# Kernel optimization log

Measured on AMD Instinct MI355X. Metric: run time of the kernel, lower is better.

The kernel has to match this reference:

```python
import jax, jax.numpy as jnp
import numpy as np

# Model dims (see init_kwargs / shape_source)
ROWS, COLS, C, K, L = 16, 16, 16, 3, 2
B, T = 16, 128
D = ROWS * COLS * C  # state_dim = 4096
PAD = (K - 1) // 2


def setup_inputs() -> dict:
    key = jax.random.key(0)
    ks = jax.random.split(key, 1 + 5 * L)
    inp = {"x_flat": jax.random.normal(ks[0], (B, T, ROWS * COLS), jnp.float32)}
    ki = 1
    for l in range(L):
        cin = (1 if l == 0 else C) + C  # conv sees concat(input, h)
        inp[f"conv_w{l}"] = jax.random.normal(ks[ki], (4 * C, cin, K), jnp.float32) * float(1.0 / np.sqrt(cin * K)); ki += 1
        inp[f"conv_b{l}"] = jnp.zeros((4 * C,), jnp.float32)
        s = float(1.0 / np.sqrt(D))
        inp[f"wq{l}"] = jax.random.normal(ks[ki], (D, D), jnp.float32) * s; ki += 1
        inp[f"wk{l}"] = jax.random.normal(ks[ki], (D, D), jnp.float32) * s; ki += 1
        inp[f"wv{l}"] = jax.random.normal(ks[ki], (D, D), jnp.float32) * s; ki += 1
        inp[f"wo{l}"] = jax.random.normal(ks[ki], (2 * D, D), jnp.float32) * float(1.0 / np.sqrt(2 * D)); ki += 1
    return inp


def _cell_step(x, h, c, cw, cb):
    # x: (B, ROWS, cin_x, COLS); h, c: (B, ROWS, C, COLS). Row-shared Conv1d
    # along cols over concat(x, h) -> 4C gates (standard ConvLSTM).
    z = jnp.concatenate([x, h], axis=2)
    z = z.reshape(B * ROWS, z.shape[2], COLS)
    g = jax.lax.conv_general_dilated(
        z, cw, window_strides=(1,), padding=[(PAD, PAD)],
        dimension_numbers=("NCH", "OIH", "NCH"))
    g = g.reshape(B, ROWS, 4 * C, COLS) + cb[None, None, :, None]
    i, f, gg, o = jnp.split(g, 4, axis=2)
    c_new = jax.nn.sigmoid(f) * c + jax.nn.sigmoid(i) * jnp.tanh(gg)
    h_new = jax.nn.sigmoid(o) * jnp.tanh(c_new)
    return h_new, c_new


def _attn_step(h_vec, kbuf, vbuf, step, wq, wo):
    # Causal dot-product attention: query from raw state, keys from raw
    # history, values from refined history (projections cached in kbuf/vbuf).
    q = h_vec @ wq                                        # (B, D)
    scores = jnp.einsum("bd,tbd->bt", q, kbuf) * (1.0 / np.sqrt(D))
    mask = (jnp.arange(T)[None, :] < step)                # (1, T) strictly-past
    scores = jnp.where(mask, scores, -1e30)
    m = jnp.max(scores, axis=1, keepdims=True)
    e = jnp.exp(scores - m) * mask
    w = e / jnp.maximum(e.sum(axis=1, keepdims=True), 1e-9)
    ctx = jnp.einsum("bt,tbd->bd", w, vbuf)               # zeros at step 0
    out = jnp.tanh(jnp.concatenate([h_vec, ctx], axis=1) @ wo)
    return out, w


def _forward(x_flat, layer_params):
    # frames: (T, B, ROWS, 1, COLS) -- matches torch view+unsqueeze(3)
    x = x_flat.reshape(B, T, ROWS, 1, COLS).transpose(1, 0, 2, 3, 4)
    h0 = tuple(jnp.zeros((B, ROWS, C, COLS), x_flat.dtype) for _ in range(L))
    kb0 = tuple(jnp.zeros((T, B, D), x_flat.dtype) for _ in range(L))

    def body(carry, x_t):
        hs, cs, kbs, vbs, s = carry
        inp = x_t
        nh, nc, nk, nv = [], [], [], []
        out = None
        for l in range(L):
            cw, cb, wq, wk, wv, wo = layer_params[l]
            h_raw, c_new = _cell_step(inp, hs[l], cs[l], cw, cb)
            h_vec = h_raw.reshape(B, D)
            out, _w = _attn_step(h_vec, kbs[l], vbs[l], s, wq, wo)
            nk.append(kbs[l].at[s].set(h_vec @ wk))   # append raw key
            nv.append(vbs[l].at[s].set(out @ wv))     # append refined value
            nh.append(h_raw); nc.append(c_new)
            inp = out.reshape(B, ROWS, C, COLS)
        return (tuple(nh), tuple(nc), tuple(nk), tuple(nv), s + 1), out

    init = (h0, h0, kb0, kb0, jnp.int32(0))
    _, outs = jax.lax.scan(body, init, x)
    return outs.transpose(1, 0, 2)  # (B, T, D) encoder outputs


def reference(x_flat, conv_w0, conv_b0, wq0, wk0, wv0, wo0,
              conv_w1, conv_b1, wq1, wk1, wv1, wo1):
    layer_params = [
        (conv_w0, conv_b0, wq0, wk0, wv0, wo0),
        (conv_w1, conv_b1, wq1, wk1, wv1, wo1),
    ]
    return _forward(x_flat, layer_params)
```

## Files before the change

### kernel.cpp

```cpp
#include <hip/hip_runtime.h>

typedef unsigned short u16;
typedef unsigned int u32;
typedef __attribute__((ext_vector_type(8))) short short8v;
typedef __attribute__((ext_vector_type(4))) float f32x4;
typedef __attribute__((ext_vector_type(8))) u16 ush8;
typedef __attribute__((ext_vector_type(4))) u16 ush4;

__device__ __forceinline__ u16 f2bf(float x) {
  u32 u = __builtin_bit_cast(u32, x);
  return (u16)((u + 0x7FFFu + ((u >> 16) & 1u)) >> 16);
}
__device__ __forceinline__ float bf2f(u16 h) {
  u32 u = ((u32)h) << 16;
  return __builtin_bit_cast(float, u);
}
__device__ __forceinline__ float sigm(float x) { return 1.f / (1.f + expf(-x)); }

typedef const __attribute__((address_space(1))) void gv_t;
typedef __attribute__((address_space(3))) void lv_t;
__device__ __forceinline__ void gload16(const void* g, void* l) {
  __builtin_amdgcn_global_load_lds((gv_t*)g, (lv_t*)l, 16, 0, 0);
}

__device__ __forceinline__ u32 ldsc32(const u32* p) {
  u32 v;
  asm volatile("global_load_dword %0, %1, off sc0 sc1\n\ts_waitcnt vmcnt(0)"
               : "=v"(v) : "v"(p) : "memory");
  return v;
}
__device__ __forceinline__ void atomswap32(u32* p, u32 v) {
  asm volatile("global_atomic_swap %0, %1, off" :: "v"(p), "v"(v) : "memory");
}

__global__ __launch_bounds__(256) void k_conv(int cin, int xmode,
    const float* __restrict__ xin, const float* __restrict__ cw,
    const float* __restrict__ cb, u16* __restrict__ hhi, u16* __restrict__ hlo)
{
  __shared__ float zb[32 * 18];
  __shared__ __align__(16) float wb[6144];
  __shared__ float bb[64];
  const int tid = threadIdx.x;
  const int b = blockIdx.x >> 4, r = blockIdx.x & 15;
  const int ch = tid >> 4, col = tid & 15;
  const int cx = cin - 16;
  for (int i = tid; i < 64 * cin * 3; i += 256) {
    int tap = i % 3, tmp = i / 3;
    int ic = tmp % cin, oc = tmp / cin;
    wb[(((oc & 15) * cin + ic) * 3 + tap) * 4 + (oc >> 4)] = cw[i];
  }
  if (tid < 64) bb[tid] = cb[tid];
  for (int i = tid; i < cin * 18; i += 256) zb[i] = 0.f;
  __syncthreads();
  float h = 0.f, c = 0.f;
  const int lane = tid & 63;
  for (int t = 0; t < 128; ++t) {
    if (xmode == 0) {
      if (ch == 0) zb[col + 1] = xin[((long)b * 128 + t) * 256 + r * 16 + col];
    } else {
      zb[ch * 18 + col + 1] = xin[((long)t * 16 + b) * 4096 + r * 256 + ch * 16 + col];
    }
    zb[(cx + ch) * 18 + col + 1] = h;
    __syncthreads();
    float a0 = bb[ch], a1 = bb[16 + ch], a2 = bb[32 + ch], a3 = bb[48 + ch];
    for (int ic = 0; ic < cin; ++ic) {
      float z1 = zb[ic * 18 + col + 1];
      float z0 = __shfl(z1, lane - 1);
      float z2 = __shfl(z1, lane + 1);
      if (col == 0) z0 = 0.f;
      if (col == 15) z2 = 0.f;
      const float4* wp = (const float4*)&wb[(ch * cin + ic) * 12];
      float4 w0 = wp[0], w1 = wp[1], w2 = wp[2];
      a0 += z0 * w0.x + z1 * w1.x + z2 * w2.x;
      a1 += z0 * w0.y + z1 * w1.y + z2 * w2.y;
      a2 += z0 * w0.z + z1 * w1.z + z2 * w2.z;
      a3 += z0 * w0.w + z1 * w1.w + z2 * w2.w;
    }
    __syncthreads();
    c = sigm(a1) * c + sigm(a0) * tanhf(a2);
    h = sigm(a3) * tanhf(c);
    long idx = ((long)t * 16 + b) * 4096 + (long)r * 256 + ch * 16 + col;
    u16 hh = f2bf(h);
    hhi[idx] = hh;
    hlo[idx] = f2bf(h - bf2f(hh));
  }
}

__global__ __launch_bounds__(256) void k_tsplit3(
    const float* __restrict__ W0, const float* __restrict__ W1,
    const float* __restrict__ W2, u16* __restrict__ hi, u16* __restrict__ lo)
{
  __shared__ float tb[32][33];
  const int y = blockIdx.y;
  const float* W = (y == 0) ? W0 : (y == 1) ? W1 : W2;
  u16* hid = hi + (unsigned long)y * 16777216UL;
  u16* lod = lo + (unsigned long)y * 16777216UL;
  const int tn = blockIdx.x & 127, tk = blockIdx.x >> 7;
  const int n0 = tn * 32, k0 = tk * 32;
  const int lr = threadIdx.x >> 5, lc = threadIdx.x & 31;
  #pragma unroll
  for (int i = 0; i < 4; ++i)
    tb[lr + i * 8][lc] = W[(long)(k0 + lr + i * 8) * 4096 + n0 + lc];
  __syncthreads();
  #pragma unroll
  for (int i = 0; i < 4; ++i) {
    int n = lr + i * 8;
    float v = tb[lc][n];
    long idx = (long)(n0 + n) * 4096 + k0 + lc;
    u16 h = f2bf(v);
    hid[idx] = h;
    lod[idx] = f2bf(v - bf2f(h));
  }
}

__global__ __launch_bounds__(256) void k_tsplit(const float* __restrict__ W,
    u16* __restrict__ hi, u16* __restrict__ lo)
{
  __shared__ float tb[32][33];
  const int tn = blockIdx.x & 127, tk = blockIdx.x >> 7;
  const int n0 = tn * 32, k0 = tk * 32;
  const int lr = threadIdx.x >> 5, lc = threadIdx.x & 31;
  #pragma unroll
  for (int i = 0; i < 4; ++i)
    tb[lr + i * 8][lc] = W[(long)(k0 + lr + i * 8) * 4096 + n0 + lc];
  __syncthreads();
  #pragma unroll
  for (int i = 0; i < 4; ++i) {
    int n = lr + i * 8;
    float v = tb[lc][n];
    long idx = (long)(n0 + n) * 4096 + k0 + lc;
    u16 h = f2bf(v);
    hi[idx] = h;
    lo[idx] = f2bf(v - bf2f(h));
  }
}

__global__ __launch_bounds__(256) void k_split(const float* __restrict__ W,
    u16* __restrict__ hi, u16* __restrict__ lo)
{
  long i = ((long)blockIdx.x * 256 + threadIdx.x) * 4;
  const float4 v = *(const float4*)&W[i];
  u16 h0 = f2bf(v.x), h1 = f2bf(v.y), h2 = f2bf(v.z), h3 = f2bf(v.w);
  ush4 hv = {h0, h1, h2, h3};
  ush4 lv = {f2bf(v.x - bf2f(h0)), f2bf(v.y - bf2f(h1)),
             f2bf(v.z - bf2f(h2)), f2bf(v.w - bf2f(h3))};
  *(ush4*)&hi[i] = hv;
  *(ush4*)&lo[i] = lv;
}

__global__ __launch_bounds__(256) void k_scores(
    const u16* __restrict__ Ahi, long lda, long aBS,
    const u16* __restrict__ Bhi, long ldb, long bBS,
    float* __restrict__ Sp)
{
  __shared__ __align__(16) u16 lds[2][16384];
  const int tid = threadIdx.x;
  const int lane = tid & 63;
  const int wv = tid >> 6;
  const long aOff = (long)blockIdx.y * aBS;
  const long bOff = (long)blockIdx.y * bBS;
  const long cOff = (long)blockIdx.y * 16384 + (long)blockIdx.z * 262144;
  const int kbase = blockIdx.z * 512;

  const int l8 = lane >> 3;
  const int cslot = (lane & 7) ^ l8;
  const int ck = (cslot & 3) * 8;
  const u16* aSrc = Ahi + aOff + (wv * 32 + l8) * lda + ck;
  const u16* bSrc = Bhi + bOff + (wv * 32 + l8) * ldb + ck;
  const int ldsAo = wv * 2048;
  const int ldsBo = 8192 + wv * 2048;

  const int r15 = lane & 15, kq = lane >> 4;
  const int s7 = r15 & 7;
  const int oHi = (kq ^ s7) * 8;
  const int aQ = (wv >> 1) * 64;
  const int bQ = (wv & 1) * 64;

  f32x4 acc[4][4] = {};

#define STAGE(buf, kofs)                                                     \
  {                                                                          \
    const u16* sa = aSrc + (kofs);                                           \
    const u16* sb = bSrc + (kofs);                                           \
    u16* la = &lds[buf][ldsAo];                                              \
    u16* lb = &lds[buf][ldsBo];                                              \
    gload16(sa,            la);        gload16(sa +  8 * lda, la + 512);     \
    gload16(sa + 16 * lda, la + 1024); gload16(sa + 24 * lda, la + 1536);    \
    gload16(sb,            lb);        gload16(sb +  8 * ldb, lb + 512);     \
    gload16(sb + 16 * ldb, lb + 1024); gload16(sb + 24 * ldb, lb + 1536);    \
  }

  STAGE(0, kbase)
  __syncthreads();
  int cur = 0;
  for (int k0 = kbase; k0 < kbase + 512; k0 += 32) {
    if (k0 + 32 < kbase + 512) STAGE(cur ^ 1, k0 + 32)
    const u16* L = &lds[cur][0];
    short8v bh[4];
    #pragma unroll
    for (int j = 0; j < 4; ++j)
      bh[j] = *(const short8v*)&L[8192 + (bQ + j * 16 + r15) * 64 + oHi];
    #pragma unroll
    for (int i = 0; i < 4; ++i) {
      short8v ah = *(const short8v*)&L[(aQ + i * 16 + r15) * 64 + oHi];
      #pragma unroll
      for (int j = 0; j < 4; ++j)
        acc[i][j] = __builtin_amdgcn_mfma_f32_16x16x32_bf16(ah, bh[j], acc[i][j], 0, 0, 0);
    }
    __syncthreads();
    cur ^= 1;
  }
#undef STAGE
  const long row0 = aQ, col0 = bQ;
  #pragma unroll
  for (int i = 0; i < 4; ++i)
    #pragma unroll
    for (int j = 0; j < 4; ++j) {
      long rr = row0 + i * 16 + kq * 4;
      long cc = col0 + j * 16 + r15;
      #pragma unroll
      for (int g = 0; g < 4; ++g)
        Sp[cOff + (rr + g) * 128 + cc] = acc[i][j][g];
    }
}

template<int NM, bool LOOUT>
__global__ __launch_bounds__(512) void k_gemm256(
    const u16* __restrict__ Ahi, const u16* __restrict__ Alo,
    const u16* __restrict__ Bhi, const u16* __restrict__ Blo,
    u16* __restrict__ Chi, u16* __restrict__ Clo, long ldc, int nTc)
{
  __shared__ __align__(16) u16 lds[73728];
  const int tid = threadIdx.x, lane = tid & 63, wv = tid >> 6;
  const int nwg = gridDim.x;
  const int bid2 = (blockIdx.x & 7) * (nwg >> 3) + (blockIdx.x >> 3);
  const int nT = bid2 % nTc, mT = bid2 / nTc;
  const long aRow0 = (long)mT * 256, bRow0 = (long)nT * 128;

  const int l8 = lane >> 3, cslot = (lane & 7) ^ l8, ck = (cslot & 3) * 8;
  const u16* aSrc = ((cslot < 4) ? Ahi : Alo) + (aRow0 + wv * 32 + l8) * 4096 + ck;
  const u16* bSrc = ((cslot < 4) ? Bhi : Blo) + (bRow0 + wv * 16 + l8) * 4096 + ck;
  const int laO = wv * 2048;
  const int lbO = 16384 + wv * 1024;

  const int r15 = lane & 15, kq = lane >> 4, s7 = r15 & 7;
  const int oHi = (kq ^ s7) * 8, oLo = ((4 + kq) ^ s7) * 8;
  const int wm = wv >> 1, wn = wv & 1;
  f32x4 acc[4][4] = {};

#define STG(buf, kofs)                                                       \
  {                                                                          \
    const u16* sa = aSrc + (kofs);                                           \
    const u16* sb = bSrc + (kofs);                                           \
    u16* la = &lds[(buf) * 24576 + laO];                                     \
    u16* lb = &lds[(buf) * 24576 + lbO];                                     \
    gload16(sa,             la);       gload16(sa +  8 * 4096, la + 512);    \
    gload16(sa + 16 * 4096, la + 1024); gload16(sa + 24 * 4096, la + 1536);  \
    gload16(sb,             lb);       gload16(sb +  8 * 4096, lb + 512);    \
  }

  STG(0, 0) STG(1, 32)
  for (int kt = 0; kt < 128; ++kt) {
    if (kt < 127) { asm volatile("s_waitcnt vmcnt(6)" ::: "memory"); }
    else          { asm volatile("s_waitcnt vmcnt(0)" ::: "memory"); }
    __builtin_amdgcn_sched_barrier(0);
    __builtin_amdgcn_s_barrier();
    const int bb = (kt % 3) * 24576;
    if (kt < 126) STG((kt + 2) % 3, (kt + 2) * 32)
    short8v ah[4], al[4], bh[4], bl[4];
    #pragma unroll
    for (int j = 0; j < 4; ++j) {
      int rb = bb + 16384 + (wn * 64 + j * 16 + r15) * 64;
      bh[j] = *(const short8v*)&lds[rb + oHi];
      if (NM >= 3) bl[j] = *(const short8v*)&lds[rb + oLo];
    }
    #pragma unroll
    for (int i = 0; i < 4; ++i) {
      int ra = bb + (wm * 64 + i * 16 + r15) * 64;
      ah[i] = *(const short8v*)&lds[ra + oHi];
      if (NM >= 2) al[i] = *(const short8v*)&lds[ra + oLo];
    }
    #pragma unroll
    for (int i = 0; i < 4; ++i)
      #pragma unroll
      for (int j = 0; j < 4; ++j) {
        acc[i][j] = __builtin_amdgcn_mfma_f32_16x16x32_bf16(ah[i], bh[j], acc[i][j], 0, 0, 0);
        if (NM >= 3) acc[i][j] = __builtin_amdgcn_mfma_f32_16x16x32_bf16(ah[i], bl[j], acc[i][j], 0, 0, 0);
        if (NM >= 2) acc[i][j] = __builtin_amdgcn_mfma_f32_16x16x32_bf16(al[i], bh[j], acc[i][j], 0, 0, 0);
      }
  }
#undef STG
  const long row0 = aRow0 + wm * 64;
  const long col0 = bRow0 + wn * 64;
  #pragma unroll
  for (int i = 0; i < 4; ++i)
    #pragma unroll
    for (int j = 0; j < 4; ++j) {
      long rr = row0 + i * 16 + kq * 4;
      long cc = col0 + j * 16 + r15;
      #pragma unroll
      for (int g = 0; g < 4; ++g) {
        float v = acc[i][j][g];
        long idx = (rr + g) * ldc + cc;
        u16 h = f2bf(v);
        Chi[idx] = h;
        if (LOOUT) Clo[idx] = f2bf(v - bf2f(h));
      }
    }
}

__global__ __launch_bounds__(256) void k_softmax(const float* __restrict__ Sp,
    float* __restrict__ Wx, u32* __restrict__ flags, u32* __restrict__ rel)
{
  if (blockIdx.x == 0) atomswap32(&flags[threadIdx.x * 16], 0);
  if (blockIdx.x == 1) atomswap32(&rel[threadIdx.x * 16], 0);
  const int wv = threadIdx.x >> 6, lane = threadIdx.x & 63;
  const int idx = blockIdx.x * 4 + wv;
  const int b = idx >> 7, t = idx & 127;
  const float* row = &Sp[(long)idx * 128];
  float s0 = 0.f, s1 = 0.f;
  #pragma unroll
  for (int s = 0; s < 8; ++s) {
    s0 += row[s * 262144 + lane];
    s1 += row[s * 262144 + lane + 64];
  }
  float v0 = (lane < t) ? s0 * 0.015625f : -1e30f;
  float v1 = (lane + 64 < t) ? s1 * 0.015625f : -1e30f;
  float m = fmaxf(v0, v1);
  #pragma unroll
  for (int off = 32; off; off >>= 1) m = fmaxf(m, __shfl_xor(m, off));
  float e0 = (lane < t) ? expf(v0 - m) : 0.f;
  float e1 = (lane + 64 < t) ? expf(v1 - m) : 0.f;
  float s = e0 + e1;
  #pragma unroll
  for (int off = 32; off; off >>= 1) s += __shfl_xor(s, off);
  float inv = 1.f / fmaxf(s, 1e-9f);
  float* wr = &Wx[((long)t * 16 + b) * 128];
  wr[lane] = e0 * inv;
  wr[lane + 64] = e1 * inv;
}

__global__ __launch_bounds__(512) void k_phaseC(
    const u16* __restrict__ Wvh, const u16* __restrict__ Wvl,
    const float* __restrict__ Wx,
    const u16* __restrict__ hoh, const u16* __restrict__ hol,
    u16* __restrict__ ring_h,
    float* __restrict__ fdest, int dmode,
    u32* __restrict__ flags, u32* __restrict__ rel)
{
  __shared__ float VO_lds[128 * 256];
  __shared__ float vo_w[8][256];
  __shared__ float pctx[2][256];
  const int tid = threadIdx.x;
  const int lane = tid & 63, wv = tid >> 6;
  const int n0 = blockIdx.x * 16;
  const int r15 = lane & 15, kq = lane >> 4;
  const long kb = (long)wv * 512 + kq * 8;

  short8v Bh[16], Bl[16];
  {
    const u16* bh = Wvh + (long)(n0 + r15) * 4096 + kb;
    const u16* bl = Wvl + (long)(n0 + r15) * 4096 + kb;
    #pragma unroll
    for (int c = 0; c < 16; ++c) {
      Bh[c] = *(const short8v*)(bh + c * 32);
      Bl[c] = *(const short8v*)(bl + c * 32);
    }
    #pragma unroll
    for (int c = 0; c < 16; ++c) {
      asm volatile("" : "+v"(Bh[c]));
      asm volatile("" : "+v"(Bl[c]));
    }
  }
  const long abase = (long)r15 * 4096 + kb;
  const int b8 = tid >> 4, col8 = tid & 15;

#define GBAR(n)                                                              \
  {                                                                          \
    asm volatile("s_waitcnt vmcnt(0)" ::: "memory");                         \
    __syncthreads();                                                         \
    if (tid == 0) {                                                          \
      atomswap32(&flags[(u32)blockIdx.x * 16], (n));                         \
      asm volatile("s_waitcnt vmcnt(0)" ::: "memory");                       \
    }                                                                        \
    if (blockIdx.x == 0) {                                                   \
      if (tid < 256) {                                                       \
        while (ldsc32(&flags[tid * 16]) < (n)) __builtin_amdgcn_s_sleep(1);  \
      }                                                                      \
      __syncthreads();                                                       \
      if (tid < 256) atomswap32(&rel[tid * 16], (n));                        \
    } else if (tid == 0) {                                                   \
      while (ldsc32(&rel[(u32)blockIdx.x * 16]) < (n))                       \
        __builtin_amdgcn_s_sleep(1);                                         \
    }                                                                        \
    __syncthreads();                                                         \
  }

#define RING_STORE(slot, oval)                                               \
  {                                                                          \
    u16 hh_ = f2bf(oval);                                                    \
    u32 vh_ = hh_;                                                           \
    u32 ph_ = (u32)__shfl_xor((int)vh_, 1);                                  \
    if (!(col8 & 1)) {                                                       \
      long oi_ = (long)(slot) * 65536 + (long)b8 * 4096 + n0 + col8;         \
      atomswap32((u32*)&ring_h[oi_], vh_ | (ph_ << 16));                     \
    }                                                                        \
  }

  if (tid < 256) {
    float v = tanhf(bf2f(hoh[(long)b8 * 12288 + n0 + col8])
                  + bf2f(hol[(long)b8 * 12288 + n0 + col8]));
    RING_STORE(0, v)
    if (dmode == 0) fdest[(long)b8 * 4096 + n0 + col8] = v;
    else            fdest[(long)b8 * 128 * 4096 + n0 + col8] = v;
  }
  u32 bn = 1;
  GBAR(bn) ++bn;

#define MF(a, b) acc = __builtin_amdgcn_mfma_f32_16x16x32_bf16(a, b, acc, 0, 0, 0);

  for (int t = 0; t < 127; ++t) {
    const u16* ph = ring_h + (long)t * 65536 + abase;
    short8v xh[16];
    #pragma unroll
    for (int c = 0; c < 16; ++c) xh[c] = *(const short8v*)(ph + c * 32);
    {
      const int p = tid >> 8, id = tid & 255;
      const int bm = id >> 4;
      const float* wrowm = &Wx[((long)(t + 1) * 16 + bm) * 128];
      float ctx = 0.f;
      for (int tp = p; tp < t; tp += 2)
        ctx += wrowm[tp] * VO_lds[tp * 256 + id];
      pctx[p][id] = ctx;
    }
    f32x4 acc = {0.f, 0.f, 0.f, 0.f};
    #pragma unroll
    for (int c = 0; c < 16; ++c) { MF(xh[c], Bh[c]) MF(xh[c], Bl[c]) }
    #pragma unroll
    for (int g = 0; g < 4; ++g)
      vo_w[wv][(kq * 4 + g) * 16 + r15] = acc[g];
    __syncthreads();
    if (tid < 256) {
      float v = vo_w[0][tid] + vo_w[1][tid] + vo_w[2][tid] + vo_w[3][tid]
              + vo_w[4][tid] + vo_w[5][tid] + vo_w[6][tid] + vo_w[7][tid];
      VO_lds[t * 256 + tid] = v;
      const float* wrow = &Wx[((long)(t + 1) * 16 + b8) * 128];
      long hix = ((long)(t + 1) * 16 + b8) * 12288 + n0 + col8;
      float o = tanhf(bf2f(hoh[hix]) + bf2f(hol[hix])
                      + pctx[0][tid] + pctx[1][tid] + wrow[t] * v);
      RING_STORE(t + 1, o)
      if (dmode == 0) fdest[((long)(t + 1) * 16 + b8) * 4096 + n0 + col8] = o;
      else            fdest[((long)b8 * 128 + (t + 1)) * 4096 + n0 + col8] = o;
    }
    if (t < 126) { GBAR(bn) ++bn; }
  }
#undef GBAR
#undef RING_STORE
#undef MF
}

extern "C" void kernel_launch(void* const* d_in, const int* in_sizes, int n_in,
                              void* d_out, int out_size, void* d_ws, size_t ws_size,
                              hipStream_t stream)
{
  (void)in_sizes; (void)n_in; (void)out_size;
  if (ws_size < 472383488UL) return;
  char* ws = (char*)d_ws;
  u16* WT_hi = (u16*)(ws + 0UL);
  u16* WT_lo = (u16*)(ws + 100663296UL);
  u16* WV_hi = (u16*)(ws + 33554432UL);
  u16* WV_lo = (u16*)(ws + 134217728UL);
  u16* QKOh  = (u16*)(ws + 201326592UL);
  u16* QKOl  = (u16*)(ws + 251658240UL);
  u16* Wvo_hi = (u16*)(ws + 301989888UL);
  u16* Wvo_lo = (u16*)(ws + 335544320UL);
  u16* Hs_hi = (u16*)(ws + 369098752UL);
  u16* Hs_lo = (u16*)(ws + 385875968UL);
  float* Wmx  = (float*)(ws + 403701760UL);
  float* OUT0 = (float*)(ws + 404754432UL);
  u16* ring_h = (u16*)(ws + 438308864UL);
  float* Sp   = (float*)(ws + 455086080UL);
  u32* flg    = (u32*)(ws + 471859200UL);
  u32* rel    = (u32*)(ws + 471875584UL);
  float* dout = (float*)d_out;
  const float* x_flat = (const float*)d_in[0];

  for (int l = 0; l < 2; ++l) {
    const float* cw = (const float*)d_in[1 + l * 6];
    const float* cb = (const float*)d_in[2 + l * 6];
    const float* wq = (const float*)d_in[3 + l * 6];
    const float* wk = (const float*)d_in[4 + l * 6];
    const float* wv = (const float*)d_in[5 + l * 6];
    const float* wo = (const float*)d_in[6 + l * 6];
    const int cin = (l == 0) ? 17 : 32;

    hipLaunchKernelGGL(k_conv, dim3(256), dim3(256), 0, stream,
        cin, l, (l == 0) ? x_flat : OUT0, cw, cb, Hs_hi, Hs_lo);

    hipLaunchKernelGGL(k_tsplit3, dim3(16384, 3), dim3(256), 0, stream,
        wq, wk, wo, WT_hi, WT_lo);
    hipLaunchKernelGGL((k_gemm256<1, false>), dim3(512), dim3(512), 0, stream,
        Hs_hi, Hs_hi, WT_hi, WT_hi, QKOh, (u16*)nullptr, 12288L, 64);
    hipLaunchKernelGGL((k_gemm256<3, true>), dim3(256), dim3(512), 0, stream,
        Hs_hi, Hs_lo, WT_hi + 33554432UL, WT_lo + 33554432UL,
        QKOh + 8192, QKOl + 8192, 12288L, 32);

    hipLaunchKernelGGL(k_tsplit, dim3(16384), dim3(256), 0, stream,
        wo + 16777216UL, WT_hi, WT_lo);
    hipLaunchKernelGGL(k_split, dim3(16384), dim3(256), 0, stream, wv, WV_hi, WV_lo);
    hipLaunchKernelGGL((k_gemm256<2, true>), dim3(512), dim3(512), 0, stream,
        WT_hi, WT_lo, WV_hi, WV_hi, Wvo_hi, Wvo_lo, 4096L, 32);

    hipLaunchKernelGGL(k_scores, dim3(1, 16, 8), dim3(256), 0, stream,
        QKOh, 12288L, 196608L, QKOh + 4096, 12288L, 196608L, Sp);
    hipLaunchKernelGGL(k_softmax, dim3(512), dim3(256), 0, stream, Sp, Wmx, flg, rel);

    hipLaunchKernelGGL(k_phaseC, dim3(256), dim3(512), 0, stream,
        Wvo_hi, Wvo_lo, Wmx, QKOh + 8192, QKOl + 8192,
        ring_h, (l == 0) ? OUT0 : dout, l, flg, rel);
  }
}
```

Before: 4.559 ms.

## Flatten grid barrier, overlap context reduction with barrier wait, merge prep kernels

The two-level grid barrier (every block signals, block 0 gathers and then broadcasts a release flag) is replaced with an all-to-all scheme in which each block polls all 256 flags directly. While the lower half of the threads spin on those flags, the upper half computes the attention context sum over past steps, moving that work off the critical path after the barrier. The wo transpose-split and wv split are also merged into one launch. The flat barrier adds polling traffic across all blocks, and the context sum now runs on only 256 threads instead of 512.

Measured after the change: 4.083 ms. 1.12x faster.

```diff
diff --git a/kernel.cpp b/kernel.cpp
--- a/kernel.cpp
+++ b/kernel.cpp
@@ -113,16 +113,29 @@
   }
 }
 
-__global__ __launch_bounds__(256) void k_tsplit(const float* __restrict__ W,
-    u16* __restrict__ hi, u16* __restrict__ lo)
-{
+__global__ __launch_bounds__(256) void k_prepB2(
+    const float* __restrict__ Woc, const float* __restrict__ Wv,
+    u16* __restrict__ thi, u16* __restrict__ tlo,
+    u16* __restrict__ vhi, u16* __restrict__ vlo)
+{
+  if (blockIdx.y == 1) {
+    long i = ((long)blockIdx.x * 256 + threadIdx.x) * 4;
+    const float4 v = *(const float4*)&Wv[i];
+    u16 h0 = f2bf(v.x), h1 = f2bf(v.y), h2 = f2bf(v.z), h3 = f2bf(v.w);
+    ush4 hv = {h0, h1, h2, h3};
+    ush4 lv = {f2bf(v.x - bf2f(h0)), f2bf(v.y - bf2f(h1)),
+               f2bf(v.z - bf2f(h2)), f2bf(v.w - bf2f(h3))};
+    *(ush4*)&vhi[i] = hv;
+    *(ush4*)&vlo[i] = lv;
+    return;
+  }
   __shared__ float tb[32][33];
   const int tn = blockIdx.x & 127, tk = blockIdx.x >> 7;
   const int n0 = tn * 32, k0 = tk * 32;
   const int lr = threadIdx.x >> 5, lc = threadIdx.x & 31;
   #pragma unroll
   for (int i = 0; i < 4; ++i)
-    tb[lr + i * 8][lc] = W[(long)(k0 + lr + i * 8) * 4096 + n0 + lc];
+    tb[lr + i * 8][lc] = Woc[(long)(k0 + lr + i * 8) * 4096 + n0 + lc];
   __syncthreads();
   #pragma unroll
   for (int i = 0; i < 4; ++i) {
@@ -130,22 +143,9 @@
     float v = tb[lc][n];
     long idx = (long)(n0 + n) * 4096 + k0 + lc;
     u16 h = f2bf(v);
-    hi[idx] = h;
-    lo[idx] = f2bf(v - bf2f(h));
-  }
-}
-
-__global__ __launch_bounds__(256) void k_split(const float* __restrict__ W,
-    u16* __restrict__ hi, u16* __restrict__ lo)
-{
-  long i = ((long)blockIdx.x * 256 + threadIdx.x) * 4;
-  const float4 v = *(const float4*)&W[i];
-  u16 h0 = f2bf(v.x), h1 = f2bf(v.y), h2 = f2bf(v.z), h3 = f2bf(v.w);
-  ush4 hv = {h0, h1, h2, h3};
-  ush4 lv = {f2bf(v.x - bf2f(h0)), f2bf(v.y - bf2f(h1)),
-             f2bf(v.z - bf2f(h2)), f2bf(v.w - bf2f(h3))};
-  *(ush4*)&hi[i] = hv;
-  *(ush4*)&lo[i] = lv;
+    thi[idx] = h;
+    tlo[idx] = f2bf(v - bf2f(h));
+  }
 }
 
 __global__ __launch_bounds__(256) void k_scores(
@@ -310,10 +310,9 @@
 }
 
 __global__ __launch_bounds__(256) void k_softmax(const float* __restrict__ Sp,
-    float* __restrict__ Wx, u32* __restrict__ flags, u32* __restrict__ rel)
+    float* __restrict__ Wx, u32* __restrict__ flags)
 {
   if (blockIdx.x == 0) atomswap32(&flags[threadIdx.x * 16], 0);
-  if (blockIdx.x == 1) atomswap32(&rel[threadIdx.x * 16], 0);
   const int wv = threadIdx.x >> 6, lane = threadIdx.x & 63;
   const int idx = blockIdx.x * 4 + wv;
   const int b = idx >> 7, t = idx & 127;
@@ -345,12 +344,11 @@
     const float* __restrict__ Wx,
     const u16* __restrict__ hoh, const u16* __restrict__ hol,
     u16* __restrict__ ring_h,
-    float* __restrict__ fdest, int dmode,
-    u32* __restrict__ flags, u32* __restrict__ rel)
+    float* __restrict__ fdest, int dmode, u32* __restrict__ flags)
 {
   __shared__ float VO_lds[128 * 256];
   __shared__ float vo_w[8][256];
-  __shared__ float pctx[2][256];
+  __shared__ float pctx0[256], pctx1[256];
   const int tid = threadIdx.x;
   const int lane = tid & 63, wv = tid >> 6;
   const int n0 = blockIdx.x * 16;
@@ -375,23 +373,25 @@
   const long abase = (long)r15 * 4096 + kb;
   const int b8 = tid >> 4, col8 = tid & 15;
 
-#define GBAR(n)                                                              \
+#define GBAR_PCTX(n, T)                                                      \
   {                                                                          \
     asm volatile("s_waitcnt vmcnt(0)" ::: "memory");                         \
     __syncthreads();                                                         \
-    if (tid == 0) {                                                          \
-      atomswap32(&flags[(u32)blockIdx.x * 16], (n));                         \
-      asm volatile("s_waitcnt vmcnt(0)" ::: "memory");                       \
-    }                                                                        \
-    if (blockIdx.x == 0) {                                                   \
-      if (tid < 256) {                                                       \
-        while (ldsc32(&flags[tid * 16]) < (n)) __builtin_amdgcn_s_sleep(1);  \
+    if (tid == 0) atomswap32(&flags[(u32)blockIdx.x * 16], (n));             \
+    if (tid >= 256) {                                                        \
+      const int id = tid - 256;                                              \
+      const int bm = id >> 4;                                                \
+      const float* wrowm = &Wx[((long)((T) + 1) * 16 + bm) * 128];           \
+      float c0 = 0.f, c1 = 0.f;                                              \
+      int tp = 0;                                                            \
+      for (; tp + 1 < (T); tp += 2) {                                        \
+        c0 += wrowm[tp] * VO_lds[tp * 256 + id];                             \
+        c1 += wrowm[tp + 1] * VO_lds[(tp + 1) * 256 + id];                   \
       }                                                                      \
-      __syncthreads();                                                       \
-      if (tid < 256) atomswap32(&rel[tid * 16], (n));                        \
-    } else if (tid == 0) {                                                   \
-      while (ldsc32(&rel[(u32)blockIdx.x * 16]) < (n))                       \
-        __builtin_amdgcn_s_sleep(1);                                         \
+      if (tp < (T)) c0 += wrowm[tp] * VO_lds[tp * 256 + id];                 \
+      pctx0[id] = c0; pctx1[id] = c1;                                        \
+    } else {                                                                 \
+      while (ldsc32(&flags[tid * 16]) < (n)) __builtin_amdgcn_s_sleep(1);    \
     }                                                                        \
     __syncthreads();                                                         \
   }
@@ -415,7 +415,7 @@
     else            fdest[(long)b8 * 128 * 4096 + n0 + col8] = v;
   }
   u32 bn = 1;
-  GBAR(bn) ++bn;
+  GBAR_PCTX(bn, 0) ++bn;
 
 #define MF(a, b) acc = __builtin_amdgcn_mfma_f32_16x16x32_bf16(a, b, acc, 0, 0, 0);
 
@@ -424,15 +424,6 @@
     short8v xh[16];
     #pragma unroll
     for (int c = 0; c < 16; ++c) xh[c] = *(const short8v*)(ph + c * 32);
-    {
-      const int p = tid >> 8, id = tid & 255;
-      const int bm = id >> 4;
-      const float* wrowm = &Wx[((long)(t + 1) * 16 + bm) * 128];
-      float ctx = 0.f;
-      for (int tp = p; tp < t; tp += 2)
-        ctx += wrowm[tp] * VO_lds[tp * 256 + id];
-      pctx[p][id] = ctx;
-    }
     f32x4 acc = {0.f, 0.f, 0.f, 0.f};
     #pragma unroll
     for (int c = 0; c < 16; ++c) { MF(xh[c], Bh[c]) MF(xh[c], Bl[c]) }
@@ -447,14 +438,14 @@
       const float* wrow = &Wx[((long)(t + 1) * 16 + b8) * 128];
       long hix = ((long)(t + 1) * 16 + b8) * 12288 + n0 + col8;
       float o = tanhf(bf2f(hoh[hix]) + bf2f(hol[hix])
-                      + pctx[0][tid] + pctx[1][tid] + wrow[t] * v);
+                      + pctx0[tid] + pctx1[tid] + wrow[t] * v);
       RING_STORE(t + 1, o)
       if (dmode == 0) fdest[((long)(t + 1) * 16 + b8) * 4096 + n0 + col8] = o;
       else            fdest[((long)b8 * 128 + (t + 1)) * 4096 + n0 + col8] = o;
     }
-    if (t < 126) { GBAR(bn) ++bn; }
-  }
-#undef GBAR
+    if (t < 126) { GBAR_PCTX(bn, t + 1) ++bn; }
+  }
+#undef GBAR_PCTX
 #undef RING_STORE
 #undef MF
 }
@@ -481,7 +472,6 @@
   u16* ring_h = (u16*)(ws + 438308864UL);
   float* Sp   = (float*)(ws + 455086080UL);
   u32* flg    = (u32*)(ws + 471859200UL);
-  u32* rel    = (u32*)(ws + 471875584UL);
   float* dout = (float*)d_out;
   const float* x_flat = (const float*)d_in[0];
 
@@ -505,18 +495,17 @@
         Hs_hi, Hs_lo, WT_hi + 33554432UL, WT_lo + 33554432UL,
         QKOh + 8192, QKOl + 8192, 12288L, 32);
 
-    hipLaunchKernelGGL(k_tsplit, dim3(16384), dim3(256), 0, stream,
-        wo + 16777216UL, WT_hi, WT_lo);
-    hipLaunchKernelGGL(k_split, dim3(16384), dim3(256), 0, stream, wv, WV_hi, WV_lo);
+    hipLaunchKernelGGL(k_prepB2, dim3(16384, 2), dim3(256), 0, stream,
+        wo + 16777216UL, wv, WT_hi, WT_lo, WV_hi, WV_lo);
     hipLaunchKernelGGL((k_gemm256<2, true>), dim3(512), dim3(512), 0, stream,
         WT_hi, WT_lo, WV_hi, WV_hi, Wvo_hi, Wvo_lo, 4096L, 32);
 
     hipLaunchKernelGGL(k_scores, dim3(1, 16, 8), dim3(256), 0, stream,
         QKOh, 12288L, 196608L, QKOh + 4096, 12288L, 196608L, Sp);
-    hipLaunchKernelGGL(k_softmax, dim3(512), dim3(256), 0, stream, Sp, Wmx, flg, rel);
+    hipLaunchKernelGGL(k_softmax, dim3(512), dim3(256), 0, stream, Sp, Wmx, flg);
 
     hipLaunchKernelGGL(k_phaseC, dim3(256), dim3(512), 0, stream,
         Wvo_hi, Wvo_lo, Wmx, QKOh + 8192, QKOl + 8192,
-        ring_h, (l == 0) ? OUT0 : dout, l, flg, rel);
-  }
-}
+        ring_h, (l == 0) ? OUT0 : dout, l, flg);
+  }
+}
```
